# Optimization experiments

Hardware: AMD Instinct MI355X
Metric: run time of the kernel (lower is better)

The kernel has to match this reference:

```python
import jax, jax.numpy as jnp
import numpy as np

B, N, C, H = 4, 2048, 768, 12


def setup_inputs() -> dict:
    key = jax.random.key(0)
    k1, k2, k3 = jax.random.split(key, 3)
    x = jax.random.normal(k1, (B, N, C), dtype=jnp.float32)
    qkv_w = jax.random.normal(k2, (3 * C, C), dtype=jnp.float32) * 0.02
    proj_w = jax.random.normal(k3, (C, C), dtype=jnp.float32) * 0.02
    proj_b = jnp.zeros((C,), dtype=jnp.float32)
    return {"x": x, "qkv_w": qkv_w, "proj_w": proj_w, "proj_b": proj_b}


def reference(x, qkv_w, proj_w, proj_b):
    b, n, c = x.shape
    hd = c // H
    scale = hd ** -0.5
    # qkv projection (no bias): (B,N,3C) -> (3,B,H,N,hd)
    qkv = (x @ qkv_w.T).reshape(b, n, 3, H, hd).transpose(2, 0, 3, 1, 4)
    q = qkv[0] * scale
    k = qkv[1]
    v = qkv[2]
    attn = jax.nn.softmax(jnp.einsum('bhqd,bhkd->bhqk', q, k), axis=-1)
    out = jnp.einsum('bhqk,bhkd->bhqd', attn, v)  # (B,H,N,hd)
    out = out.transpose(0, 2, 1, 3).reshape(b, n, c)
    return out @ proj_w.T + proj_b
```

## Files before the change

kernel.cpp:

```cpp
#include <hip/hip_runtime.h>

#define B_SZ 4
#define SEQ  2048
#define CH   768
#define NH   12
#define HD   64

typedef float f32x4  __attribute__((ext_vector_type(4)));
typedef __bf16 bf16x8 __attribute__((ext_vector_type(8)));
typedef __bf16 bf16x2 __attribute__((ext_vector_type(2)));

#define MFMA16(a,b,c) __builtin_amdgcn_mfma_f32_16x16x32_bf16(a,b,c,0,0,0)

#define QSCALE 0.1803368801111204f

#if __has_builtin(__builtin_amdgcn_exp2f)
#define EXP2(x) __builtin_amdgcn_exp2f(x)
#else
#define EXP2(x) exp2f(x)
#endif

__device__ __forceinline__ unsigned pack2(float a, float b) {
    union { bf16x2 v; unsigned u; } p;
    p.v[0] = (__bf16)a; p.v[1] = (__bf16)b;
    return p.u;
}

__device__ __forceinline__ void lds_dma16(const void* g, void* l) {
    __builtin_amdgcn_global_load_lds(
        (const __attribute__((address_space(1))) void*)g,
        (__attribute__((address_space(3))) void*)(unsigned)(unsigned long long)l,
        16, 0, 0);
}

__global__ __launch_bounds__(256) void convert_bf16(const float* __restrict__ src,
                                                    __bf16* __restrict__ dst, int n) {
    int i = (blockIdx.x * 256 + threadIdx.x) * 4;
    if (i >= n) return;
    float4 v = *(const float4*)(src + i);
    union { __bf16 h[4]; uint2 u; } o;
    o.h[0] = (__bf16)v.x; o.h[1] = (__bf16)v.y; o.h[2] = (__bf16)v.z; o.h[3] = (__bf16)v.w;
    *(uint2*)(dst + i) = o.u;
}

__device__ __forceinline__ void gemm128_loop(const __bf16* __restrict__ A,
                                             const __bf16* __restrict__ Bm,
                                             int K, int rowBlk, int colBlk,
                                             __bf16* As, __bf16* Bs,
                                             f32x4 acc[4][4]) {
    const int tid  = threadIdx.x;
    const int lane = tid & 63, wid = tid >> 6;
    const int quad = lane >> 4, l16 = lane & 15;
    const int wm = wid >> 1, wn = wid & 1;

    f32x4 z = {0.f, 0.f, 0.f, 0.f};
#pragma unroll
    for (int mi = 0; mi < 4; ++mi)
#pragma unroll
        for (int ni = 0; ni < 4; ++ni) acc[mi][ni] = z;

    for (int k0 = 0; k0 < K; k0 += 64) {
        __syncthreads();
#pragma unroll
        for (int i = 0; i < 4; ++i) {
            int s = i * 256 + tid;
            int row = s >> 3, pc = s & 7;
            int lc = pc ^ (row & 7);
            lds_dma16(A  + (size_t)(rowBlk + row) * K + k0 + lc * 8, As + s * 8);
            lds_dma16(Bm + (size_t)(colBlk + row) * K + k0 + lc * 8, Bs + s * 8);
        }
        __syncthreads();

#pragma unroll
        for (int kc = 0; kc < 2; ++kc) {
            bf16x8 af[4], bfr[4];
#pragma unroll
            for (int mi = 0; mi < 4; ++mi) {
                int row = wm * 64 + mi * 16 + l16;
                int pc = (quad + 4 * kc) ^ (row & 7);
                af[mi] = *(const bf16x8*)(As + row * 64 + pc * 8);
            }
#pragma unroll
            for (int ni = 0; ni < 4; ++ni) {
                int row = wn * 64 + ni * 16 + l16;
                int pc = (quad + 4 * kc) ^ (row & 7);
                bfr[ni] = *(const bf16x8*)(Bs + row * 64 + pc * 8);
            }
#pragma unroll
            for (int mi = 0; mi < 4; ++mi)
#pragma unroll
                for (int ni = 0; ni < 4; ++ni)
                    acc[mi][ni] = MFMA16(af[mi], bfr[ni], acc[mi][ni]);
        }
    }
}

__global__ __launch_bounds__(256) void qkv_gemm(const __bf16* __restrict__ Xb,
                                                const __bf16* __restrict__ Wb,
                                                __bf16* __restrict__ Qb,
                                                __bf16* __restrict__ Kb,
                                                __bf16* __restrict__ Vt) {
    __shared__ __bf16 smem[128 * 128];
    f32x4 acc[4][4];
    const int rowBlk = blockIdx.x * 128, colBlk = blockIdx.y * 128;
    gemm128_loop(Xb, Wb, CH, rowBlk, colBlk, smem, smem + 128 * 64, acc);

    const int tid = threadIdx.x;
    const int lane = tid & 63, wid = tid >> 6;
    const int quad = lane >> 4, l16 = lane & 15, wm = wid >> 1, wn = wid & 1;
    const int b = rowBlk >> 11, n0 = rowBlk & (SEQ - 1);

    if (colBlk < 2 * CH) {
        const int isK = (colBlk >= CH);
#pragma unroll
        for (int mi = 0; mi < 4; ++mi)
#pragma unroll
            for (int ni = 0; ni < 4; ++ni)
#pragma unroll
                for (int r = 0; r < 4; ++r) {
                    int n = n0 + wm * 64 + mi * 16 + quad * 4 + r;
                    int cc = colBlk - (isK ? CH : 0) + wn * 64 + ni * 16 + l16;
                    int h = cc >> 6, d = cc & 63;
                    size_t idx = (size_t)((b * NH + h) * SEQ + n) * HD + d;
                    float v = acc[mi][ni][r];
                    if (isK) Kb[idx] = (__bf16)v;
                    else     Qb[idx] = (__bf16)(v * QSCALE);
                }
    } else {
        const int vblk = colBlk - 2 * CH;
        __syncthreads();
#pragma unroll
        for (int mi = 0; mi < 4; ++mi)
#pragma unroll
            for (int ni = 0; ni < 4; ++ni)
#pragma unroll
                for (int r = 0; r < 4; ++r) {
                    int rl = wm * 64 + mi * 16 + quad * 4 + r;
                    int cl = wn * 64 + ni * 16 + l16;
                    smem[cl * 128 + (((rl >> 3) ^ (cl & 15)) << 3) + (rl & 7)] =
                        (__bf16)acc[mi][ni][r];
                }
        __syncthreads();
        const int dl = tid >> 1;
        const int d  = vblk + dl;
        const int h  = d >> 6, dd = d & 63;
        const size_t base = (size_t)((b * NH + h) * HD + dd) * SEQ + n0;
#pragma unroll
        for (int j2 = 0; j2 < 8; ++j2) {
            int j = (tid & 1) * 8 + j2;
            uint4 val = *(const uint4*)(smem + dl * 128 + ((j ^ (dl & 15)) << 3));
            *(uint4*)(Vt + base + j * 8) = val;
        }
    }
}

__global__ __launch_bounds__(256, 5) void flash_attn(const __bf16* __restrict__ Qb,
                                                     const __bf16* __restrict__ Kb,
                                                     const __bf16* __restrict__ Vt,
                                                     __bf16* __restrict__ Ab) {
    __shared__ __bf16 smem[2][64 * 64];
    __bf16* Ks = smem[0];
    __bf16* Vs = smem[1];

    const int tid  = threadIdx.x;
    const int lane = tid & 63, wid = tid >> 6;
    const int quad = lane >> 4, l16 = lane & 15;

    const int lin  = blockIdx.x;
    const int xcd  = lin & 7, idx = lin >> 3;
    const int bh   = xcd * 6 + (idx >> 5);
    const int qblk = idx & 31;
    const int b    = bh / NH, head = bh - b * NH;

    const int q = qblk * 64 + wid * 16 + l16;

    bf16x8 qf[2];
#pragma unroll
    for (int kcd = 0; kcd < 2; ++kcd)
        qf[kcd] = *(const bf16x8*)(Qb + (size_t)(bh * SEQ + q) * HD + kcd * 32 + quad * 8);

    const int key_e = ((l16 >> 2) << 3) + (l16 & 3);
    const int key_o = ((((l16 >> 2) ^ 1)) << 3) + 4 + (l16 & 3);

    f32x4 ot[4];
    f32x4 z = {0.f, 0.f, 0.f, 0.f};
#pragma unroll
    for (int dg = 0; dg < 4; ++dg) ot[dg] = z;
    float l_part = 0.f;

    const __bf16* Kbh = Kb + (size_t)bh * SEQ * HD;
    const __bf16* Vbh = Vt + (size_t)bh * HD * SEQ;

    const int s_row = tid >> 3, s_pc = tid & 7;
    const int s_lc0 = s_pc ^ (s_row & 7);
    const int s_lc1 = s_pc ^ ((s_row + 32) & 7);

    for (int kb = 0; kb < SEQ / 64; ++kb) {
        const int kbase = kb * 64;
        __syncthreads();
        lds_dma16(Kbh + (size_t)(kbase + s_row) * HD + s_lc0 * 8,      Ks + tid * 8);
        lds_dma16(Kbh + (size_t)(kbase + s_row + 32) * HD + s_lc1 * 8, Ks + 2048 + tid * 8);
        lds_dma16(Vbh + (size_t)s_row * SEQ + kbase + s_lc0 * 8,       Vs + tid * 8);
        lds_dma16(Vbh + (size_t)(s_row + 32) * SEQ + kbase + s_lc1 * 8, Vs + 2048 + tid * 8);
        __syncthreads();

        f32x4 st[4];
#pragma unroll
        for (int g = 0; g < 4; ++g) {
            st[g] = z;
            const int key = ((g >> 1) << 5) + ((g & 1) ? key_o : key_e);
#pragma unroll
            for (int kcd = 0; kcd < 2; ++kcd) {
                int c8 = quad + (kcd << 2);
                bf16x8 kf = *(const bf16x8*)(Ks + key * 64 + ((c8 ^ (key & 7)) << 3));
                st[g] = MFMA16(kf, qf[kcd], st[g]);
            }
        }

#pragma unroll
        for (int g = 0; g < 4; ++g)
#pragma unroll
            for (int r = 0; r < 4; ++r) {
                float p = EXP2(st[g][r]);
                st[g][r] = p;
                l_part += p;
            }

        bf16x8 pf[2];
#pragma unroll
        for (int kk = 0; kk < 2; ++kk) {
            unsigned w0 = pack2(st[2 * kk][0], st[2 * kk][1]);
            unsigned w1 = pack2(st[2 * kk][2], st[2 * kk][3]);
            unsigned x0 = pack2(st[2 * kk + 1][0], st[2 * kk + 1][1]);
            unsigned x1 = pack2(st[2 * kk + 1][2], st[2 * kk + 1][3]);
            unsigned w2 = (unsigned)__shfl_xor((int)x0, 16, 64);
            unsigned w3 = (unsigned)__shfl_xor((int)x1, 16, 64);
            union { bf16x8 v; unsigned u[4]; } f;
            f.u[0] = w0; f.u[1] = w1; f.u[2] = w2; f.u[3] = w3;
            pf[kk] = f.v;
        }

#pragma unroll
        for (int dg = 0; dg < 4; ++dg)
#pragma unroll
            for (int kk = 0; kk < 2; ++kk) {
                int row = (dg << 4) + l16;
                int c8 = quad + (kk << 2);
                bf16x8 vf = *(const bf16x8*)(Vs + row * 64 + ((c8 ^ (row & 7)) << 3));
                ot[dg] = MFMA16(vf, pf[kk], ot[dg]);
            }
    }

    l_part += __shfl_xor(l_part, 16, 64);
    l_part += __shfl_xor(l_part, 32, 64);
    const float rinv = 1.f / l_part;

    __syncthreads();
    __bf16 (*Ob)[72] = (__bf16(*)[72])&smem[0][0];
#pragma unroll
    for (int dg = 0; dg < 4; ++dg)
#pragma unroll
        for (int r = 0; r < 4; ++r) {
            int d = (dg << 4) + (quad << 2) + r;
            Ob[wid * 16 + l16][d] = (__bf16)(ot[dg][r] * rinv);
        }
    __syncthreads();
    {
        const int ql = tid >> 2, c0 = (tid & 3) * 16;
        uint4 v0 = *(const uint4*)(&Ob[ql][c0]);
        uint4 v1 = *(const uint4*)(&Ob[ql][c0 + 8]);
        __bf16* dst = Ab + (size_t)(b * SEQ + qblk * 64 + ql) * CH + head * HD + c0;
        *(uint4*)(dst)     = v0;
        *(uint4*)(dst + 8) = v1;
    }
}

__global__ __launch_bounds__(256) void proj_gemm(const __bf16* __restrict__ Ab,
                                                 const __bf16* __restrict__ Pw,
                                                 const float* __restrict__ bias,
                                                 float* __restrict__ out) {
    __shared__ __bf16 As[128 * 64];
    __shared__ __bf16 Bs[128 * 64];
    f32x4 acc[4][4];
    const int rowBlk = blockIdx.x * 128, colBlk = blockIdx.y * 128;
    gemm128_loop(Ab, Pw, CH, rowBlk, colBlk, As, Bs, acc);

    const int lane = threadIdx.x & 63, wid = threadIdx.x >> 6;
    const int quad = lane >> 4, l16 = lane & 15, wm = wid >> 1, wn = wid & 1;
#pragma unroll
    for (int mi = 0; mi < 4; ++mi)
#pragma unroll
        for (int ni = 0; ni < 4; ++ni)
#pragma unroll
            for (int r = 0; r < 4; ++r) {
                int row = rowBlk + wm * 64 + mi * 16 + quad * 4 + r;
                int col = colBlk + wn * 64 + ni * 16 + l16;
                out[(size_t)row * CH + col] = acc[mi][ni][r] + bias[col];
            }
}

extern "C" void kernel_launch(void* const* d_in, const int* in_sizes, int n_in,
                              void* d_out, int out_size, void* d_ws, size_t ws_size,
                              hipStream_t stream) {
    const float* x      = (const float*)d_in[0];
    const float* qkv_w  = (const float*)d_in[1];
    const float* proj_w = (const float*)d_in[2];
    const float* proj_b = (const float*)d_in[3];
    float* out = (float*)d_out;

    char* ws = (char*)d_ws;
    const size_t nX = (size_t)B_SZ * SEQ * CH;
    const size_t nW = (size_t)3 * CH * CH;
    const size_t nP = (size_t)CH * CH;
    const size_t nQ = (size_t)B_SZ * NH * SEQ * HD;

    __bf16* Xb = (__bf16*)(ws);
    __bf16* Wb = (__bf16*)(ws + 2 * nX);
    __bf16* Pw = (__bf16*)(ws + 2 * (nX + nW));
    __bf16* Qb = (__bf16*)(ws + 2 * (nX + nW + nP));
    __bf16* Kb = (__bf16*)(ws + 2 * (nX + nW + nP + nQ));
    __bf16* Vt = (__bf16*)(ws + 2 * (nX + nW + nP + 2 * nQ));
    __bf16* Ab = (__bf16*)(ws + 2 * (nX + nW + nP + 3 * nQ));

    convert_bf16<<<(int)(nX / 1024), 256, 0, stream>>>(x, Xb, (int)nX);
    convert_bf16<<<(int)(nW / 1024), 256, 0, stream>>>(qkv_w, Wb, (int)nW);
    convert_bf16<<<(int)(nP / 1024), 256, 0, stream>>>(proj_w, Pw, (int)nP);

    qkv_gemm<<<dim3((B_SZ * SEQ) / 128, (3 * CH) / 128), 256, 0, stream>>>(Xb, Wb, Qb, Kb, Vt);

    flash_attn<<<1536, 256, 0, stream>>>(Qb, Kb, Vt, Ab);

    proj_gemm<<<dim3((B_SZ * SEQ) / 128, CH / 128), 256, 0, stream>>>(Ab, Pw, proj_b, out);
}
```

Measured before the change: 226.1 us.

## Process two query tiles per flash-attention block to reuse K/V loads

New measurement: 215.5 us. 1.05x faster.

```diff
diff --git a/kernel.cpp b/kernel.cpp
--- a/kernel.cpp
+++ b/kernel.cpp
@@ -19,6 +19,8 @@
 #else
 #define EXP2(x) exp2f(x)
 #endif
+
+#define SWZ(row) (((row) ^ ((row) >> 3)) & 7)
 
 __device__ __forceinline__ unsigned pack2(float a, float b) {
     union { bf16x2 v; unsigned u; } p;
@@ -154,13 +156,13 @@
     }
 }
 
-__global__ __launch_bounds__(256, 5) void flash_attn(const __bf16* __restrict__ Qb,
+__global__ __launch_bounds__(256, 3) void flash_attn(const __bf16* __restrict__ Qb,
                                                      const __bf16* __restrict__ Kb,
                                                      const __bf16* __restrict__ Vt,
                                                      __bf16* __restrict__ Ab) {
-    __shared__ __bf16 smem[2][64 * 64];
-    __bf16* Ks = smem[0];
-    __bf16* Vs = smem[1];
+    __shared__ __bf16 smem[9216];
+    __bf16* Ks = smem;
+    __bf16* Vs = smem + 4096;
 
     const int tid  = threadIdx.x;
     const int lane = tid & 63, wid = tid >> 6;
@@ -168,76 +170,100 @@
 
     const int lin  = blockIdx.x;
     const int xcd  = lin & 7, idx = lin >> 3;
-    const int bh   = xcd * 6 + (idx >> 5);
-    const int qblk = idx & 31;
+    const int bh   = xcd * 6 + (idx >> 4);
+    const int qblk = idx & 15;
     const int b    = bh / NH, head = bh - b * NH;
 
-    const int q = qblk * 64 + wid * 16 + l16;
-
-    bf16x8 qf[2];
-#pragma unroll
-    for (int kcd = 0; kcd < 2; ++kcd)
-        qf[kcd] = *(const bf16x8*)(Qb + (size_t)(bh * SEQ + q) * HD + kcd * 32 + quad * 8);
+    const int qA = qblk * 128 + wid * 16 + l16;
+    const int qB = qA + 64;
+
+    bf16x8 qfA[2], qfB[2];
+#pragma unroll
+    for (int kcd = 0; kcd < 2; ++kcd) {
+        qfA[kcd] = *(const bf16x8*)(Qb + (size_t)(bh * SEQ + qA) * HD + kcd * 32 + quad * 8);
+        qfB[kcd] = *(const bf16x8*)(Qb + (size_t)(bh * SEQ + qB) * HD + kcd * 32 + quad * 8);
+    }
 
     const int key_e = ((l16 >> 2) << 3) + (l16 & 3);
     const int key_o = ((((l16 >> 2) ^ 1)) << 3) + 4 + (l16 & 3);
 
-    f32x4 ot[4];
+    f32x4 otA[4], otB[4];
     f32x4 z = {0.f, 0.f, 0.f, 0.f};
 #pragma unroll
-    for (int dg = 0; dg < 4; ++dg) ot[dg] = z;
-    float l_part = 0.f;
+    for (int dg = 0; dg < 4; ++dg) { otA[dg] = z; otB[dg] = z; }
+    float lA = 0.f, lB = 0.f;
 
     const __bf16* Kbh = Kb + (size_t)bh * SEQ * HD;
     const __bf16* Vbh = Vt + (size_t)bh * HD * SEQ;
 
     const int s_row = tid >> 3, s_pc = tid & 7;
-    const int s_lc0 = s_pc ^ (s_row & 7);
-    const int s_lc1 = s_pc ^ ((s_row + 32) & 7);
+    const int s_lc0 = s_pc ^ SWZ(s_row);
+    const int s_lc1 = s_pc ^ SWZ(s_row + 32);
 
     for (int kb = 0; kb < SEQ / 64; ++kb) {
         const int kbase = kb * 64;
         __syncthreads();
-        lds_dma16(Kbh + (size_t)(kbase + s_row) * HD + s_lc0 * 8,      Ks + tid * 8);
-        lds_dma16(Kbh + (size_t)(kbase + s_row + 32) * HD + s_lc1 * 8, Ks + 2048 + tid * 8);
-        lds_dma16(Vbh + (size_t)s_row * SEQ + kbase + s_lc0 * 8,       Vs + tid * 8);
+        lds_dma16(Kbh + (size_t)(kbase + s_row) * HD + s_lc0 * 8,       Ks + tid * 8);
+        lds_dma16(Kbh + (size_t)(kbase + s_row + 32) * HD + s_lc1 * 8,  Ks + 2048 + tid * 8);
+        lds_dma16(Vbh + (size_t)s_row * SEQ + kbase + s_lc0 * 8,        Vs + tid * 8);
         lds_dma16(Vbh + (size_t)(s_row + 32) * SEQ + kbase + s_lc1 * 8, Vs + 2048 + tid * 8);
         __syncthreads();
 
-        f32x4 st[4];
+        f32x4 stA[4], stB[4];
+#pragma unroll
+        for (int g = 0; g < 4; ++g) { stA[g] = z; stB[g] = z; }
 #pragma unroll
         for (int g = 0; g < 4; ++g) {
-            st[g] = z;
             const int key = ((g >> 1) << 5) + ((g & 1) ? key_o : key_e);
 #pragma unroll
             for (int kcd = 0; kcd < 2; ++kcd) {
                 int c8 = quad + (kcd << 2);
-                bf16x8 kf = *(const bf16x8*)(Ks + key * 64 + ((c8 ^ (key & 7)) << 3));
-                st[g] = MFMA16(kf, qf[kcd], st[g]);
-            }
-        }
-
+                bf16x8 kf = *(const bf16x8*)(Ks + key * 64 + ((c8 ^ SWZ(key)) << 3));
+                stA[g] = MFMA16(kf, qfA[kcd], stA[g]);
+                stB[g] = MFMA16(kf, qfB[kcd], stB[g]);
+            }
+        }
+
+        bf16x8 pfA[2], pfB[2];
 #pragma unroll
         for (int g = 0; g < 4; ++g)
 #pragma unroll
             for (int r = 0; r < 4; ++r) {
-                float p = EXP2(st[g][r]);
-                st[g][r] = p;
-                l_part += p;
-            }
-
-        bf16x8 pf[2];
+                float p = EXP2(stA[g][r]);
+                stA[g][r] = p;
+                lA += p;
+            }
 #pragma unroll
         for (int kk = 0; kk < 2; ++kk) {
-            unsigned w0 = pack2(st[2 * kk][0], st[2 * kk][1]);
-            unsigned w1 = pack2(st[2 * kk][2], st[2 * kk][3]);
-            unsigned x0 = pack2(st[2 * kk + 1][0], st[2 * kk + 1][1]);
-            unsigned x1 = pack2(st[2 * kk + 1][2], st[2 * kk + 1][3]);
+            unsigned w0 = pack2(stA[2 * kk][0], stA[2 * kk][1]);
+            unsigned w1 = pack2(stA[2 * kk][2], stA[2 * kk][3]);
+            unsigned x0 = pack2(stA[2 * kk + 1][0], stA[2 * kk + 1][1]);
+            unsigned x1 = pack2(stA[2 * kk + 1][2], stA[2 * kk + 1][3]);
             unsigned w2 = (unsigned)__shfl_xor((int)x0, 16, 64);
             unsigned w3 = (unsigned)__shfl_xor((int)x1, 16, 64);
             union { bf16x8 v; unsigned u[4]; } f;
             f.u[0] = w0; f.u[1] = w1; f.u[2] = w2; f.u[3] = w3;
-            pf[kk] = f.v;
+            pfA[kk] = f.v;
+        }
+#pragma unroll
+        for (int g = 0; g < 4; ++g)
+#pragma unroll
+            for (int r = 0; r < 4; ++r) {
+                float p = EXP2(stB[g][r]);
+                stB[g][r] = p;
+                lB += p;
+            }
+#pragma unroll
+        for (int kk = 0; kk < 2; ++kk) {
+            unsigned w0 = pack2(stB[2 * kk][0], stB[2 * kk][1]);
+            unsigned w1 = pack2(stB[2 * kk][2], stB[2 * kk][3]);
+            unsigned x0 = pack2(stB[2 * kk + 1][0], stB[2 * kk + 1][1]);
+            unsigned x1 = pack2(stB[2 * kk + 1][2], stB[2 * kk + 1][3]);
+            unsigned w2 = (unsigned)__shfl_xor((int)x0, 16, 64);
+            unsigned w3 = (unsigned)__shfl_xor((int)x1, 16, 64);
+            union { bf16x8 v; unsigned u[4]; } f;
+            f.u[0] = w0; f.u[1] = w1; f.u[2] = w2; f.u[3] = w3;
+            pfB[kk] = f.v;
         }
 
 #pragma unroll
@@ -246,32 +272,35 @@
             for (int kk = 0; kk < 2; ++kk) {
                 int row = (dg << 4) + l16;
                 int c8 = quad + (kk << 2);
-                bf16x8 vf = *(const bf16x8*)(Vs + row * 64 + ((c8 ^ (row & 7)) << 3));
-                ot[dg] = MFMA16(vf, pf[kk], ot[dg]);
-            }
-    }
-
-    l_part += __shfl_xor(l_part, 16, 64);
-    l_part += __shfl_xor(l_part, 32, 64);
-    const float rinv = 1.f / l_part;
+                bf16x8 vf = *(const bf16x8*)(Vs + row * 64 + ((c8 ^ SWZ(row)) << 3));
+                otA[dg] = MFMA16(vf, pfA[kk], otA[dg]);
+                otB[dg] = MFMA16(vf, pfB[kk], otB[dg]);
+            }
+    }
+
+    lA += __shfl_xor(lA, 16, 64);
+    lA += __shfl_xor(lA, 32, 64);
+    lB += __shfl_xor(lB, 16, 64);
+    lB += __shfl_xor(lB, 32, 64);
+    const float rA = 1.f / lA, rB = 1.f / lB;
 
     __syncthreads();
-    __bf16 (*Ob)[72] = (__bf16(*)[72])&smem[0][0];
+    __bf16 (*Ob)[72] = (__bf16(*)[72])smem;
 #pragma unroll
     for (int dg = 0; dg < 4; ++dg)
 #pragma unroll
         for (int r = 0; r < 4; ++r) {
             int d = (dg << 4) + (quad << 2) + r;
-            Ob[wid * 16 + l16][d] = (__bf16)(ot[dg][r] * rinv);
+            Ob[wid * 16 + l16][d]      = (__bf16)(otA[dg][r] * rA);
+            Ob[64 + wid * 16 + l16][d] = (__bf16)(otB[dg][r] * rB);
         }
     __syncthreads();
     {
-        const int ql = tid >> 2, c0 = (tid & 3) * 16;
-        uint4 v0 = *(const uint4*)(&Ob[ql][c0]);
-        uint4 v1 = *(const uint4*)(&Ob[ql][c0 + 8]);
-        __bf16* dst = Ab + (size_t)(b * SEQ + qblk * 64 + ql) * CH + head * HD + c0;
-        *(uint4*)(dst)     = v0;
-        *(uint4*)(dst + 8) = v1;
+        const int row = tid >> 1, c0 = (tid & 1) * 32;
+        __bf16* dst = Ab + (size_t)(b * SEQ + qblk * 128 + row) * CH + head * HD + c0;
+#pragma unroll
+        for (int j = 0; j < 4; ++j)
+            *(uint4*)(dst + j * 8) = *(const uint4*)(&Ob[row][c0 + j * 8]);
     }
 }
 
@@ -328,7 +357,7 @@
 
     qkv_gemm<<<dim3((B_SZ * SEQ) / 128, (3 * CH) / 128), 256, 0, stream>>>(Xb, Wb, Qb, Kb, Vt);
 
-    flash_attn<<<1536, 256, 0, stream>>>(Qb, Kb, Vt, Ab);
+    flash_attn<<<768, 256, 0, stream>>>(Qb, Kb, Vt, Ab);
 
     proj_gemm<<<dim3((B_SZ * SEQ) / 128, CH / 128), 256, 0, stream>>>(Ab, Pw, proj_b, out);
 }
```
